# Performance work log

Hardware: AMD Instinct MI355X
Metric: run time of the kernel (lower is better)

## Reference

```python
import jax, jax.numpy as jnp
import numpy as np

WAY = 5
SHOT = 5
NEIGHBOR_K = 3


def setup_inputs() -> dict:
    key = jax.random.key(0)
    k1, k2 = jax.random.split(key)
    x1 = jax.random.normal(k1, (75, 640, 21, 21), dtype=jnp.float32)   # queries
    x2 = jax.random.normal(k2, (25, 640, 21, 21), dtype=jnp.float32)   # support (way*shot)
    return {"x1": x1, "x2": x2}


def reference(x1, x2):
    Q, C, H, W = x1.shape
    S = x2.shape[0]  # way * shot
    HW = H * W

    # queries: [Q, C, HW] -> [Q, HW, C], L2-normalize each local descriptor
    q = jnp.transpose(x1.reshape(Q, C, HW), (0, 2, 1))
    q = q / jnp.linalg.norm(q, axis=2, keepdims=True)

    # support: [S, HW, C], normalize, regroup per class: [way, shot*HW, C]
    s = jnp.transpose(x2.reshape(S, C, HW), (0, 2, 1))
    s = s / jnp.linalg.norm(s, axis=2, keepdims=True)
    s = s.reshape(WAY, SHOT * HW, C)

    # cosine similarity of every query descriptor vs every class descriptor
    # [Q, way, HW, shot*HW]
    sim = jnp.einsum('qmc,wnc->qwmn', q, s)

    # top-k neighbors per query descriptor along class-descriptor axis, then sum
    topk_vals, _ = jax.lax.top_k(sim, NEIGHBOR_K)   # [Q, way, HW, k]
    img2class_sim = jnp.sum(topk_vals, axis=(2, 3))  # [Q, way]
    return img2class_sim
```

## Files before the change

### kernel.cpp

```cpp
#include <hip/hip_runtime.h>

typedef unsigned char u8;
typedef float f32x4 __attribute__((ext_vector_type(4)));

#define C_DIM 640
#define HW_DIM 441
#define QN 75
#define SN 25
#define WAYS 5
#define MROWS 33075
#define MCH   96
#define MBLK  345
#define MPAD  33120
#define NWAY  2205
#define NPAD  2304
#define BN    384
#define NT    6
#define SCL   16.0f
#define INV_SCL2 (1.0f / (SCL * SCL))

__device__ __forceinline__ void glds16(const void* g, void* l) {
  __builtin_amdgcn_global_load_lds(
      (__attribute__((address_space(1))) unsigned int*)g,
      (__attribute__((address_space(3))) unsigned int*)l, 16, 0, 0);
}

__device__ __forceinline__ unsigned pk4_fp8(float a, float b, float c, float d) {
  unsigned v = 0;
  v = __builtin_amdgcn_cvt_pk_fp8_f32(a, b, v, false);
  v = __builtin_amdgcn_cvt_pk_fp8_f32(c, d, v, true);
  return v;
}

__global__ void zero_pad(u8* __restrict__ A8, u8* __restrict__ S8,
                         float* __restrict__ out) {
  int i = blockIdx.x * 256 + threadIdx.x;
  if (i < 28800) {
    A8[(size_t)MROWS * C_DIM + i] = 0;
    return;
  }
  i -= 28800;
  if (i < 316800) {
    const int w = i / 63360;
    const int r = i % 63360;
    S8[((size_t)w * NPAD + NWAY) * C_DIM + r] = 0;
    return;
  }
  i -= 316800;
  if (i < QN * WAYS) out[i] = 0.f;
}

__global__ __launch_bounds__(256)
void prep_norm_transpose(const float* __restrict__ src, u8* __restrict__ dst,
                         int support) {
  const int bid = blockIdx.x;
  const int img = bid / 7;
  const int mt = bid % 7;
  const int m0 = mt * 64;
  const int t = threadIdx.x;
  const int mloc = t & 63;
  const int cpart = t >> 6;
  const int m = m0 + mloc;
  const int m_eff = (m < HW_DIM) ? m : (HW_DIM - 1);
  const float* base = src + (size_t)img * (C_DIM * HW_DIM);

  float ss = 0.f;
  const int c0 = cpart * 160;
  for (int c = c0; c < c0 + 160; ++c) {
    float v = base[(size_t)c * HW_DIM + m_eff];
    ss += v * v;
  }
  __shared__ float red[256];
  __shared__ float inv[64];
  red[t] = ss;
  __syncthreads();
  if (t < 64) {
    float s4 = red[t] + red[t + 64] + red[t + 128] + red[t + 192];
    inv[t] = rsqrtf(s4) * SCL;
  }
  __syncthreads();

  size_t drow0;
  if (support) {
    const int w = img / 5, shot = img % 5;
    drow0 = (size_t)w * NPAD + (size_t)shot * HW_DIM;
  } else {
    drow0 = (size_t)img * HW_DIM;
  }

  __shared__ __align__(16) u8 T[64][80];
  const float iv = inv[mloc];
  const int mw = t >> 2;
  const int cg = t & 3;
  const int m_out = m0 + mw;

  for (int ct = 0; ct < 10; ++ct) {
    float f[16];
#pragma unroll
    for (int ci = 0; ci < 16; ++ci) {
      const int c = ct * 64 + cpart * 16 + ci;
      f[ci] = base[(size_t)c * HW_DIM + m_eff] * iv;
    }
    __syncthreads();
    uint4 w;
    w.x = pk4_fp8(f[0], f[1], f[2], f[3]);
    w.y = pk4_fp8(f[4], f[5], f[6], f[7]);
    w.z = pk4_fp8(f[8], f[9], f[10], f[11]);
    w.w = pk4_fp8(f[12], f[13], f[14], f[15]);
    *(uint4*)&T[mloc][cpart * 16] = w;
    __syncthreads();
    if (m_out < HW_DIM) {
      const uint4 v = *(const uint4*)&T[mw][cg * 16];
      *(uint4*)(dst + (drow0 + m_out) * C_DIM + ct * 64 + cg * 16) = v;
    }
  }
}

__global__ __launch_bounds__(512, 2)
void simtopk(const u8* __restrict__ A8, const u8* __restrict__ S8,
             float* __restrict__ out) {
  __shared__ __align__(16) u8 As[MCH * C_DIM];
  __shared__ __align__(16) u8 Bs[2][BN * 128];
  __shared__ float qsum[2];

  const int bid = blockIdx.x;
  const int way = bid / MBLK;
  const int mc = bid % MBLK;
  const int R0 = mc * MCH;
  const int tid = threadIdx.x;
  const int lane = tid & 63;
  const int wv = tid >> 6;
  const int wm = (wv >> 2) * 48;
  const int wn = (wv & 3) * 96;
  const int l15 = lane & 15;
  const int l4 = lane >> 4;

  if (tid < 2) qsum[tid] = 0.f;

  const u8* Sway = S8 + (size_t)way * NPAD * C_DIM;
  const u8* Ab = A8 + (size_t)R0 * C_DIM;

#pragma unroll
  for (int i = 0; i < 8; ++i) {
    const int id = wv * 8 + i;
    if (id < 60) {
      const int oct = id / 5, i2 = id % 5;
      const int lin = i2 * 64 + lane;
      const int row = lin / 40;
      const int quad = lin % 40;
      const int sq = (quad & ~7) | ((quad & 7) ^ (row & 7));
      glds16(Ab + (unsigned)oct * 5120 + (unsigned)(row * 640 + sq * 16),
             As + oct * 5120 + i2 * 1024);
    }
  }

  const unsigned brow =
      (unsigned)((lane >> 3) * 640 + (((lane & 7) ^ (lane >> 3)) * 16));
#pragma unroll
  for (int j = 0; j < 6; ++j) {
    const int st = wv * 6 + j;
    glds16(Sway + (unsigned)st * (8 * 640) + brow, Bs[0] + st * 1024);
  }

  int aBase[3][4], bBase[6][4];
#pragma unroll
  for (int s = 0; s < 4; ++s) {
    const int phys = ((2 * s + (l4 >> 1)) ^ (l15 & 7)) * 16 + (l4 & 1) * 8;
#pragma unroll
    for (int mi = 0; mi < 3; ++mi)
      aBase[mi][s] = (wm + mi * 16 + l15) * 640 + phys;
#pragma unroll
    for (int ni = 0; ni < 6; ++ni)
      bBase[ni][s] = (wn + ni * 16 + l15) * 128 + phys;
  }

  f32x4 acc[3][6];
  const f32x4 z4 = {0.f, 0.f, 0.f, 0.f};
#pragma unroll
  for (int mi = 0; mi < 3; ++mi)
#pragma unroll
    for (int ni = 0; ni < 6; ++ni) acc[mi][ni] = z4;

  float t0[12], t1[12], t2[12];
#pragma unroll
  for (int r = 0; r < 12; ++r) { t0[r] = -1e30f; t1[r] = -1e30f; t2[r] = -1e30f; }

  int p = 0;
  for (int nt = 0; nt < NT; ++nt) {
#pragma unroll
    for (int kt = 0; kt < 5; ++kt) {
      __syncthreads();

      if (!(nt == NT - 1 && kt == 4)) {
        const int nt1 = (kt == 4) ? nt + 1 : nt;
        const int kt1 = (kt == 4) ? 0 : kt + 1;
        const unsigned off =
            (unsigned)nt1 * (BN * C_DIM) + (unsigned)(kt1 * 128);
#pragma unroll
        for (int j = 0; j < 6; ++j) {
          const int st = wv * 6 + j;
          glds16(Sway + (unsigned)st * (8 * 640) + brow + off,
                 Bs[p ^ 1] + st * 1024);
        }
      }

      const u8* Bp = Bs[p];
      long long af[3][4];
#pragma unroll
      for (int mi = 0; mi < 3; ++mi)
#pragma unroll
        for (int s = 0; s < 4; ++s)
          af[mi][s] = *(const long long*)(As + aBase[mi][s] + kt * 128);

#pragma unroll
      for (int ni = 0; ni < 6; ++ni) {
        long long bf[4];
#pragma unroll
        for (int s = 0; s < 4; ++s)
          bf[s] = *(const long long*)(Bp + bBase[ni][s]);
#pragma unroll
        for (int s = 0; s < 4; ++s)
#pragma unroll
          for (int mi = 0; mi < 3; ++mi)
            acc[mi][ni] = __builtin_amdgcn_mfma_f32_16x16x32_fp8_fp8(
                af[mi][s], bf[s], acc[mi][ni], 0, 0, 0);
      }
      p ^= 1;
    }

    const bool lastTile = (nt == NT - 1);
#pragma unroll
    for (int ni = 0; ni < 6; ++ni) {
      const int ncol = nt * BN + wn + ni * 16 + l15;
      const bool bad = lastTile && (ncol >= NWAY);
#pragma unroll
      for (int mi = 0; mi < 3; ++mi)
#pragma unroll
        for (int i = 0; i < 4; ++i) {
          float v = acc[mi][ni][i];
          if (bad) v = -1e30f;
          const int r = mi * 4 + i;
          t2[r] = fmaxf(t2[r], fminf(v, t1[r]));
          t1[r] = fmaxf(t1[r], fminf(v, t0[r]));
          t0[r] = fmaxf(t0[r], v);
          acc[mi][ni][i] = 0.f;
        }
    }
  }

#pragma unroll
  for (int d = 1; d <= 8; d <<= 1) {
#pragma unroll
    for (int r = 0; r < 12; ++r) {
      const float o0 = __shfl_xor(t0[r], d);
      const float o1 = __shfl_xor(t1[r], d);
      const float o2 = __shfl_xor(t2[r], d);
      t2[r] = fmaxf(t2[r], fminf(o0, t1[r]));
      t1[r] = fmaxf(t1[r], fminf(o0, t0[r]));
      t0[r] = fmaxf(t0[r], o0);
      t2[r] = fmaxf(t2[r], fminf(o1, t1[r]));
      t1[r] = fmaxf(t1[r], fminf(o1, t0[r]));
      t0[r] = fmaxf(t0[r], o1);
      t2[r] = fmaxf(t2[r], fminf(o2, t1[r]));
      t1[r] = fmaxf(t1[r], fminf(o2, t0[r]));
      t0[r] = fmaxf(t0[r], o2);
    }
  }

  __syncthreads();
  float* part = (float*)&Bs[0][0];
  if (l15 == 0) {
    const int nq = wv & 3;
#pragma unroll
    for (int r = 0; r < 12; ++r) {
      const int mi = r >> 2, i = r & 3;
      const int row_local = wm + mi * 16 + l4 * 4 + i;
      part[(nq * MCH + row_local) * 4 + 0] = t0[r];
      part[(nq * MCH + row_local) * 4 + 1] = t1[r];
      part[(nq * MCH + row_local) * 4 + 2] = t2[r];
    }
  }
  __syncthreads();
  if (tid < MCH) {
    const int grow = R0 + tid;
    if (grow < MROWS) {
      float a0 = part[tid * 4 + 0], a1 = part[tid * 4 + 1], a2 = part[tid * 4 + 2];
#pragma unroll
      for (int nq = 1; nq < 4; ++nq) {
        const float b0 = part[(nq * MCH + tid) * 4 + 0];
        const float b1 = part[(nq * MCH + tid) * 4 + 1];
        const float b2 = part[(nq * MCH + tid) * 4 + 2];
        a2 = fmaxf(a2, fminf(b0, a1)); a1 = fmaxf(a1, fminf(b0, a0)); a0 = fmaxf(a0, b0);
        a2 = fmaxf(a2, fminf(b1, a1)); a1 = fmaxf(a1, fminf(b1, a0)); a0 = fmaxf(a0, b1);
        a2 = fmaxf(a2, fminf(b2, a1)); a1 = fmaxf(a1, fminf(b2, a0)); a0 = fmaxf(a0, b2);
      }
      const float rs = (a0 + a1 + a2) * INV_SCL2;
      const int qq = grow / HW_DIM;
      atomicAdd(&qsum[qq - (R0 / HW_DIM)], rs);
    }
  }
  __syncthreads();
  if (tid < 2) {
    const int qq = R0 / HW_DIM + tid;
    if (qq < QN) atomicAdd(out + qq * WAYS + way, qsum[tid]);
  }
}

extern "C" void kernel_launch(void* const* d_in, const int* in_sizes, int n_in,
                              void* d_out, int out_size, void* d_ws, size_t ws_size,
                              hipStream_t stream) {
  const float* x1 = (const float*)d_in[0];
  const float* x2 = (const float*)d_in[1];
  float* out = (float*)d_out;
  u8* A8 = (u8*)d_ws;
  u8* S8 = (u8*)d_ws + (size_t)MPAD * C_DIM;

  hipLaunchKernelGGL(zero_pad, dim3(1352), dim3(256), 0, stream, A8, S8, out);
  hipLaunchKernelGGL(prep_norm_transpose, dim3(QN * 7), dim3(256), 0, stream,
                     x1, A8, 0);
  hipLaunchKernelGGL(prep_norm_transpose, dim3(SN * 7), dim3(256), 0, stream,
                     x2, S8, 1);
  hipLaunchKernelGGL(simtopk, dim3(WAYS * MBLK), dim3(512), 0, stream,
                     A8, S8, out);
}
```

Baseline: 634.5 us.

## Switch similarity GEMM to int8 32x32x32 MFMA with integer top-k

```diff
diff --git a/kernel.cpp b/kernel.cpp
--- a/kernel.cpp
+++ b/kernel.cpp
@@ -1,7 +1,8 @@
 #include <hip/hip_runtime.h>
 
 typedef unsigned char u8;
-typedef float f32x4 __attribute__((ext_vector_type(4)));
+typedef int i32x4 __attribute__((ext_vector_type(4)));
+typedef int i32x16 __attribute__((ext_vector_type(16)));
 
 #define C_DIM 640
 #define HW_DIM 441
@@ -9,15 +10,15 @@
 #define SN 25
 #define WAYS 5
 #define MROWS 33075
-#define MCH   96
-#define MBLK  345
-#define MPAD  33120
+#define MCH   128
+#define MBLK  259
+#define MPAD  33152
 #define NWAY  2205
 #define NPAD  2304
-#define BN    384
-#define NT    6
-#define SCL   16.0f
-#define INV_SCL2 (1.0f / (SCL * SCL))
+#define BN    256
+#define NT    9
+#define INV_Q2 (1.0f / 16129.0f)
+#define NEGINF (-2147483647 - 1)
 
 __device__ __forceinline__ void glds16(const void* g, void* l) {
   __builtin_amdgcn_global_load_lds(
@@ -25,21 +26,14 @@
       (__attribute__((address_space(3))) unsigned int*)l, 16, 0, 0);
 }
 
-__device__ __forceinline__ unsigned pk4_fp8(float a, float b, float c, float d) {
-  unsigned v = 0;
-  v = __builtin_amdgcn_cvt_pk_fp8_f32(a, b, v, false);
-  v = __builtin_amdgcn_cvt_pk_fp8_f32(c, d, v, true);
-  return v;
-}
-
 __global__ void zero_pad(u8* __restrict__ A8, u8* __restrict__ S8,
                          float* __restrict__ out) {
   int i = blockIdx.x * 256 + threadIdx.x;
-  if (i < 28800) {
+  if (i < 49280) {
     A8[(size_t)MROWS * C_DIM + i] = 0;
     return;
   }
-  i -= 28800;
+  i -= 49280;
   if (i < 316800) {
     const int w = i / 63360;
     const int r = i % 63360;
@@ -76,7 +70,7 @@
   __syncthreads();
   if (t < 64) {
     float s4 = red[t] + red[t + 64] + red[t + 128] + red[t + 192];
-    inv[t] = rsqrtf(s4) * SCL;
+    inv[t] = rsqrtf(s4) * 127.0f;
   }
   __syncthreads();
 
@@ -95,18 +89,18 @@
   const int m_out = m0 + mw;
 
   for (int ct = 0; ct < 10; ++ct) {
-    float f[16];
+    int q[16];
 #pragma unroll
     for (int ci = 0; ci < 16; ++ci) {
       const int c = ct * 64 + cpart * 16 + ci;
-      f[ci] = base[(size_t)c * HW_DIM + m_eff] * iv;
+      q[ci] = __float2int_rn(base[(size_t)c * HW_DIM + m_eff] * iv);
     }
     __syncthreads();
     uint4 w;
-    w.x = pk4_fp8(f[0], f[1], f[2], f[3]);
-    w.y = pk4_fp8(f[4], f[5], f[6], f[7]);
-    w.z = pk4_fp8(f[8], f[9], f[10], f[11]);
-    w.w = pk4_fp8(f[12], f[13], f[14], f[15]);
+    w.x = (q[0] & 255) | ((q[1] & 255) << 8) | ((q[2] & 255) << 16) | ((q[3] & 255) << 24);
+    w.y = (q[4] & 255) | ((q[5] & 255) << 8) | ((q[6] & 255) << 16) | ((q[7] & 255) << 24);
+    w.z = (q[8] & 255) | ((q[9] & 255) << 8) | ((q[10] & 255) << 16) | ((q[11] & 255) << 24);
+    w.w = (q[12] & 255) | ((q[13] & 255) << 8) | ((q[14] & 255) << 16) | ((q[15] & 255) << 24);
     *(uint4*)&T[mloc][cpart * 16] = w;
     __syncthreads();
     if (m_out < HW_DIM) {
@@ -130,10 +124,10 @@
   const int tid = threadIdx.x;
   const int lane = tid & 63;
   const int wv = tid >> 6;
-  const int wm = (wv >> 2) * 48;
-  const int wn = (wv & 3) * 96;
-  const int l15 = lane & 15;
-  const int l4 = lane >> 4;
+  const int wmB = (wv >> 2) * 64;
+  const int wnB = (wv & 3) * 64;
+  const int r5 = lane & 31;
+  const int h = lane >> 5;
 
   if (tid < 2) qsum[tid] = 0.f;
 
@@ -141,49 +135,48 @@
   const u8* Ab = A8 + (size_t)R0 * C_DIM;
 
 #pragma unroll
-  for (int i = 0; i < 8; ++i) {
-    const int id = wv * 8 + i;
-    if (id < 60) {
-      const int oct = id / 5, i2 = id % 5;
-      const int lin = i2 * 64 + lane;
-      const int row = lin / 40;
-      const int quad = lin % 40;
-      const int sq = (quad & ~7) | ((quad & 7) ^ (row & 7));
-      glds16(Ab + (unsigned)oct * 5120 + (unsigned)(row * 640 + sq * 16),
-             As + oct * 5120 + i2 * 1024);
-    }
+  for (int i = 0; i < 10; ++i) {
+    const int id = wv * 10 + i;
+    const int oct = id / 5, i2 = id % 5;
+    const int lin = i2 * 64 + lane;
+    const int row = lin / 40;
+    const int quad = lin % 40;
+    const int sq = (quad & ~7) | ((quad & 7) ^ (row & 7));
+    glds16(Ab + (unsigned)(oct * 5120 + row * 640 + sq * 16),
+           As + oct * 5120 + i2 * 1024);
   }
 
   const unsigned brow =
       (unsigned)((lane >> 3) * 640 + (((lane & 7) ^ (lane >> 3)) * 16));
 #pragma unroll
-  for (int j = 0; j < 6; ++j) {
-    const int st = wv * 6 + j;
+  for (int j = 0; j < 4; ++j) {
+    const int st = wv * 4 + j;
     glds16(Sway + (unsigned)st * (8 * 640) + brow, Bs[0] + st * 1024);
   }
 
-  int aBase[3][4], bBase[6][4];
+  int aAddr[2][4], bAddr[2][4];
 #pragma unroll
   for (int s = 0; s < 4; ++s) {
-    const int phys = ((2 * s + (l4 >> 1)) ^ (l15 & 7)) * 16 + (l4 & 1) * 8;
-#pragma unroll
-    for (int mi = 0; mi < 3; ++mi)
-      aBase[mi][s] = (wm + mi * 16 + l15) * 640 + phys;
-#pragma unroll
-    for (int ni = 0; ni < 6; ++ni)
-      bBase[ni][s] = (wn + ni * 16 + l15) * 128 + phys;
-  }
-
-  f32x4 acc[3][6];
-  const f32x4 z4 = {0.f, 0.f, 0.f, 0.f};
-#pragma unroll
-  for (int mi = 0; mi < 3; ++mi)
-#pragma unroll
-    for (int ni = 0; ni < 6; ++ni) acc[mi][ni] = z4;
-
-  float t0[12], t1[12], t2[12];
-#pragma unroll
-  for (int r = 0; r < 12; ++r) { t0[r] = -1e30f; t1[r] = -1e30f; t2[r] = -1e30f; }
+    const int pq = ((2 * s + h) ^ (r5 & 7)) * 16;
+#pragma unroll
+    for (int mi = 0; mi < 2; ++mi)
+      aAddr[mi][s] = (wmB + mi * 32 + r5) * 640 + pq;
+#pragma unroll
+    for (int ni = 0; ni < 2; ++ni)
+      bAddr[ni][s] = (wnB + ni * 32 + r5) * 128 + pq;
+  }
+
+  i32x16 acc[2][2];
+#pragma unroll
+  for (int mi = 0; mi < 2; ++mi)
+#pragma unroll
+    for (int ni = 0; ni < 2; ++ni)
+#pragma unroll
+      for (int g = 0; g < 16; ++g) acc[mi][ni][g] = 0;
+
+  int t0[32], t1[32], t2[32];
+#pragma unroll
+  for (int r = 0; r < 32; ++r) { t0[r] = NEGINF; t1[r] = NEGINF; t2[r] = NEGINF; }
 
   int p = 0;
   for (int nt = 0; nt < NT; ++nt) {
@@ -197,104 +190,96 @@
         const unsigned off =
             (unsigned)nt1 * (BN * C_DIM) + (unsigned)(kt1 * 128);
 #pragma unroll
-        for (int j = 0; j < 6; ++j) {
-          const int st = wv * 6 + j;
+        for (int j = 0; j < 4; ++j) {
+          const int st = wv * 4 + j;
           glds16(Sway + (unsigned)st * (8 * 640) + brow + off,
                  Bs[p ^ 1] + st * 1024);
         }
       }
 
       const u8* Bp = Bs[p];
-      long long af[3][4];
-#pragma unroll
-      for (int mi = 0; mi < 3; ++mi)
-#pragma unroll
-        for (int s = 0; s < 4; ++s)
-          af[mi][s] = *(const long long*)(As + aBase[mi][s] + kt * 128);
-
-#pragma unroll
-      for (int ni = 0; ni < 6; ++ni) {
-        long long bf[4];
-#pragma unroll
-        for (int s = 0; s < 4; ++s)
-          bf[s] = *(const long long*)(Bp + bBase[ni][s]);
-#pragma unroll
-        for (int s = 0; s < 4; ++s)
-#pragma unroll
-          for (int mi = 0; mi < 3; ++mi)
-            acc[mi][ni] = __builtin_amdgcn_mfma_f32_16x16x32_fp8_fp8(
-                af[mi][s], bf[s], acc[mi][ni], 0, 0, 0);
+      const int ka = kt * 128;
+#pragma unroll
+      for (int s = 0; s < 4; ++s) {
+        const i32x4 a0 = *(const i32x4*)(As + aAddr[0][s] + ka);
+        const i32x4 a1 = *(const i32x4*)(As + aAddr[1][s] + ka);
+        const i32x4 b0 = *(const i32x4*)(Bp + bAddr[0][s]);
+        const i32x4 b1 = *(const i32x4*)(Bp + bAddr[1][s]);
+        acc[0][0] = __builtin_amdgcn_mfma_i32_32x32x32_i8(a0, b0, acc[0][0], 0, 0, 0);
+        acc[1][0] = __builtin_amdgcn_mfma_i32_32x32x32_i8(a1, b0, acc[1][0], 0, 0, 0);
+        acc[0][1] = __builtin_amdgcn_mfma_i32_32x32x32_i8(a0, b1, acc[0][1], 0, 0, 0);
+        acc[1][1] = __builtin_amdgcn_mfma_i32_32x32x32_i8(a1, b1, acc[1][1], 0, 0, 0);
       }
       p ^= 1;
     }
 
-    const bool lastTile = (nt == NT - 1);
-#pragma unroll
-    for (int ni = 0; ni < 6; ++ni) {
-      const int ncol = nt * BN + wn + ni * 16 + l15;
-      const bool bad = lastTile && (ncol >= NWAY);
-#pragma unroll
-      for (int mi = 0; mi < 3; ++mi)
-#pragma unroll
-        for (int i = 0; i < 4; ++i) {
-          float v = acc[mi][ni][i];
-          if (bad) v = -1e30f;
-          const int r = mi * 4 + i;
-          t2[r] = fmaxf(t2[r], fminf(v, t1[r]));
-          t1[r] = fmaxf(t1[r], fminf(v, t0[r]));
-          t0[r] = fmaxf(t0[r], v);
-          acc[mi][ni][i] = 0.f;
+    const bool lastT = (nt == NT - 1);
+#pragma unroll
+    for (int ni = 0; ni < 2; ++ni) {
+      const int ncol = nt * BN + wnB + ni * 32 + r5;
+      const bool bad = lastT && (ncol >= NWAY);
+#pragma unroll
+      for (int mi = 0; mi < 2; ++mi)
+#pragma unroll
+        for (int g = 0; g < 16; ++g) {
+          int v = acc[mi][ni][g];
+          if (bad) v = NEGINF;
+          const int r = mi * 16 + g;
+          t2[r] = max(t2[r], min(v, t1[r]));
+          t1[r] = max(t1[r], min(v, t0[r]));
+          t0[r] = max(t0[r], v);
+          acc[mi][ni][g] = 0;
         }
     }
   }
 
 #pragma unroll
-  for (int d = 1; d <= 8; d <<= 1) {
-#pragma unroll
-    for (int r = 0; r < 12; ++r) {
-      const float o0 = __shfl_xor(t0[r], d);
-      const float o1 = __shfl_xor(t1[r], d);
-      const float o2 = __shfl_xor(t2[r], d);
-      t2[r] = fmaxf(t2[r], fminf(o0, t1[r]));
-      t1[r] = fmaxf(t1[r], fminf(o0, t0[r]));
-      t0[r] = fmaxf(t0[r], o0);
-      t2[r] = fmaxf(t2[r], fminf(o1, t1[r]));
-      t1[r] = fmaxf(t1[r], fminf(o1, t0[r]));
-      t0[r] = fmaxf(t0[r], o1);
-      t2[r] = fmaxf(t2[r], fminf(o2, t1[r]));
-      t1[r] = fmaxf(t1[r], fminf(o2, t0[r]));
-      t0[r] = fmaxf(t0[r], o2);
-    }
-  }
-
-  __syncthreads();
-  float* part = (float*)&Bs[0][0];
-  if (l15 == 0) {
+  for (int d = 1; d <= 2; d <<= 1) {
+#pragma unroll
+    for (int r = 0; r < 32; ++r) {
+      const int o0 = __shfl_xor(t0[r], d);
+      const int o1 = __shfl_xor(t1[r], d);
+      const int o2 = __shfl_xor(t2[r], d);
+      t2[r] = max(t2[r], min(o0, t1[r]));
+      t1[r] = max(t1[r], min(o0, t0[r]));
+      t0[r] = max(t0[r], o0);
+      t2[r] = max(t2[r], min(o1, t1[r]));
+      t1[r] = max(t1[r], min(o1, t0[r]));
+      t0[r] = max(t0[r], o1);
+      t2[r] = max(t2[r], min(o2, t1[r]));
+      t1[r] = max(t1[r], min(o2, t0[r]));
+      t0[r] = max(t0[r], o2);
+    }
+  }
+
+  __syncthreads();
+  int* part = (int*)&Bs[0][0];
+  if ((r5 & 3) == 0) {
     const int nq = wv & 3;
-#pragma unroll
-    for (int r = 0; r < 12; ++r) {
-      const int mi = r >> 2, i = r & 3;
-      const int row_local = wm + mi * 16 + l4 * 4 + i;
-      part[(nq * MCH + row_local) * 4 + 0] = t0[r];
-      part[(nq * MCH + row_local) * 4 + 1] = t1[r];
-      part[(nq * MCH + row_local) * 4 + 2] = t2[r];
+    const int grp = nq * 8 + (r5 >> 2);
+#pragma unroll
+    for (int r = 0; r < 32; ++r) {
+      const int mi = r >> 4, g = r & 15;
+      const int row_local = wmB + mi * 32 + (g & 3) + 8 * (g >> 2) + 4 * h;
+      i32x4 v;
+      v[0] = t0[r]; v[1] = t1[r]; v[2] = t2[r]; v[3] = NEGINF;
+      *(i32x4*)&part[(row_local * 32 + grp) * 4] = v;
     }
   }
   __syncthreads();
   if (tid < MCH) {
     const int grow = R0 + tid;
     if (grow < MROWS) {
-      float a0 = part[tid * 4 + 0], a1 = part[tid * 4 + 1], a2 = part[tid * 4 + 2];
-#pragma unroll
-      for (int nq = 1; nq < 4; ++nq) {
-        const float b0 = part[(nq * MCH + tid) * 4 + 0];
-        const float b1 = part[(nq * MCH + tid) * 4 + 1];
-        const float b2 = part[(nq * MCH + tid) * 4 + 2];
-        a2 = fmaxf(a2, fminf(b0, a1)); a1 = fmaxf(a1, fminf(b0, a0)); a0 = fmaxf(a0, b0);
-        a2 = fmaxf(a2, fminf(b1, a1)); a1 = fmaxf(a1, fminf(b1, a0)); a0 = fmaxf(a0, b1);
-        a2 = fmaxf(a2, fminf(b2, a1)); a1 = fmaxf(a1, fminf(b2, a0)); a0 = fmaxf(a0, b2);
+      int a0 = NEGINF, a1 = NEGINF, a2 = NEGINF;
+#pragma unroll 4
+      for (int j = 0; j < 32; ++j) {
+        const int jj = (j + tid) & 31;
+        const i32x4 v = *(const i32x4*)&part[(tid * 32 + jj) * 4];
+        a2 = max(a2, min(v[0], a1)); a1 = max(a1, min(v[0], a0)); a0 = max(a0, v[0]);
+        a2 = max(a2, min(v[1], a1)); a1 = max(a1, min(v[1], a0)); a0 = max(a0, v[1]);
+        a2 = max(a2, min(v[2], a1)); a1 = max(a1, min(v[2], a0)); a0 = max(a0, v[2]);
       }
-      const float rs = (a0 + a1 + a2) * INV_SCL2;
+      const float rs = (float)(a0 + a1 + a2) * INV_Q2;
       const int qq = grow / HW_DIM;
       atomicAdd(&qsum[qq - (R0 / HW_DIM)], rs);
     }
@@ -315,7 +300,7 @@
   u8* A8 = (u8*)d_ws;
   u8* S8 = (u8*)d_ws + (size_t)MPAD * C_DIM;
 
-  hipLaunchKernelGGL(zero_pad, dim3(1352), dim3(256), 0, stream, A8, S8, out);
+  hipLaunchKernelGGL(zero_pad, dim3(1432), dim3(256), 0, stream, A8, S8, out);
   hipLaunchKernelGGL(prep_norm_transpose, dim3(QN * 7), dim3(256), 0, stream,
                      x1, A8, 0);
   hipLaunchKernelGGL(prep_norm_transpose, dim3(SN * 7), dim3(256), 0, stream,
```

Measured after the change: 560.3 us. -11.7%, faster.
